# Performance work log

Measured on AMD Instinct MI355X. Metric: run time of the kernel, lower is better.

Reference implementation:

```python
import jax, jax.numpy as jnp
import numpy as np

H = 8        # heads
DH = 64      # dim_head
EPS = 1e-5   # LayerNorm eps (torch default)


def setup_inputs() -> dict:
    key = jax.random.key(0)
    k0, k1, k2, k3, k4 = jax.random.split(key, 5)
    b, l, n, dim = 2, 8, 256, 512
    inner = H * DH
    return {
        "xyzs": jax.random.normal(k0, (b, l, n, 3), dtype=jnp.float32),
        "features": jax.random.normal(k1, (b, l, n, dim), dtype=jnp.float32),
        "ln_gamma": jnp.ones((dim,), dtype=jnp.float32),
        "ln_beta": jnp.zeros((dim,), dtype=jnp.float32),
        "w_qkv": jax.random.normal(k2, (dim, 3 * inner), dtype=jnp.float32) * 0.02,
        "w_sp": jax.random.normal(k3, (3, DH), dtype=jnp.float32) * 0.3,
        "w_out": jax.random.normal(k4, (inner, dim), dtype=jnp.float32) * 0.02,
        "b_out": jnp.zeros((dim,), dtype=jnp.float32),
    }


def reference(xyzs, features, ln_gamma, ln_beta, w_qkv, w_sp, w_out, b_out):
    b, l, n, dim = features.shape
    m = l * n
    inner = H * DH
    scale = DH ** (-0.5)

    # LayerNorm over last dim (biased variance, eps=1e-5)
    mu = jnp.mean(features, axis=-1, keepdims=True)
    var = jnp.var(features, axis=-1, keepdims=True)
    normed = (features - mu) * jax.lax.rsqrt(var + EPS) * ln_gamma + ln_beta

    # qkv projection, chunk into q,k,v, reshape 'b l n (h d) -> b h (l n) d'
    qkv = normed.reshape(b, m, dim) @ w_qkv            # [b, m, 3*inner]
    def split_heads(t):
        return t.reshape(b, m, H, DH).transpose(0, 2, 1, 3)  # [b, h, m, d]
    q = split_heads(qkv[..., :inner])
    k = split_heads(qkv[..., inner:2 * inner])
    v = split_heads(qkv[..., 2 * inner:])

    dots = jnp.einsum('bhid,bhjd->bhij', q, k) * scale  # [b, h, m, m]
    attn = jax.nn.softmax(dots, axis=-1)
    v_out = jnp.einsum('bhij,bhjd->bhid', attn, v)      # [b, h, m, d]

    # pairwise coordinate deltas: delta[b,i,j,c] = xyz[b,j,c] - xyz[b,i,c]
    xyz_f = xyzs.reshape(b, m, 3)
    delta = xyz_f[:, None, :, :] - xyz_f[:, :, None, :]  # [b, m, m, 3]
    # attention-weighted aggregation over j (avoids [b,h,m,m,3] intermediate)
    agg = jnp.einsum('bhij,bijc->bhic', attn, delta)     # [b, h, m, 3]
    disp = agg @ w_sp                                    # [b, h, m, DH]

    out = v_out + disp                                   # [b, h, m, DH]
    out = out.transpose(0, 2, 1, 3).reshape(b, m, inner) # 'b h m d -> b m (h d)'
    out = jax.nn.gelu(out @ w_out + b_out, approximate=False)
    return out.reshape(b, l, n, dim) + features
```

## Files before the change

kernel.cpp:

```cpp
#include <hip/hip_runtime.h>
#include <hip/hip_bf16.h>
#include <math.h>

#define BB   2
#define MM   2048
#define DIM  512
#define NH   8
#define DHd  64
#define NQK  1536
#define ROWS 4096
#define NROW 32768

typedef __hip_bfloat16 bf16;
typedef __attribute__((ext_vector_type(8))) short bf16x8;
typedef __attribute__((ext_vector_type(4))) float f32x4;
typedef __attribute__((ext_vector_type(8))) unsigned short us8;

__device__ __forceinline__ unsigned short f2bf_bits(float x) {
    bf16 h = __float2bfloat16(x);
    return *(unsigned short*)&h;
}
__device__ __forceinline__ float bf2f(unsigned short u) {
    unsigned int v = ((unsigned int)u) << 16;
    return __uint_as_float(v);
}

__global__ __launch_bounds__(256) void pre_kernel(
    const float* __restrict__ feat, const float* __restrict__ gamma,
    const float* __restrict__ beta, unsigned short* __restrict__ normed,
    const float* __restrict__ wqkv, const float* __restrict__ wout,
    unsigned short* __restrict__ wqkvT, unsigned short* __restrict__ woutT)
{
    __shared__ float st[64][65];
    int b = blockIdx.x;
    int tid = threadIdx.x;
    if (b < ROWS) {
        const float* fr = feat + (size_t)b * DIM;
        float x0 = fr[tid];
        float x1 = fr[tid + 256];
        float s  = x0 + x1;
        float ss = x0 * x0 + x1 * x1;
        #pragma unroll
        for (int o = 32; o >= 1; o >>= 1) { s += __shfl_down(s, o); ss += __shfl_down(ss, o); }
        __shared__ float ws_[4], wss_[4];
        int wid = tid >> 6, lane = tid & 63;
        if (lane == 0) { ws_[wid] = s; wss_[wid] = ss; }
        __syncthreads();
        if (tid == 0) {
            float a = 0.f, c = 0.f;
            for (int i = 0; i < 4; i++) { a += ws_[i]; c += wss_[i]; }
            ws_[0] = a; wss_[0] = c;
        }
        __syncthreads();
        float mu  = ws_[0] * (1.0f / DIM);
        float var = wss_[0] * (1.0f / DIM) - mu * mu;
        float inv = rsqrtf(var + 1e-5f);
        normed[(size_t)b * DIM + tid]       = f2bf_bits((x0 - mu) * inv * gamma[tid] + beta[tid]);
        normed[(size_t)b * DIM + tid + 256] = f2bf_bits((x1 - mu) * inv * gamma[tid + 256] + beta[tid + 256]);
        return;
    }
    int idx = b - ROWS;
    const float* in; unsigned short* out; int N, n0;
    if (idx < 192) { in = wqkv; out = wqkvT; N = NQK; n0 = (idx >> 3) * 64; }
    else { idx -= 192; in = wout; out = woutT; N = DIM; n0 = (idx >> 3) * 64; }
    int k0 = (idx & 7) * 64;
    #pragma unroll
    for (int p = 0; p < 16; p++) {
        int e = tid + p * 256;
        int r = e >> 6, c = e & 63;
        st[r][c] = in[(size_t)(k0 + r) * N + n0 + c];
    }
    __syncthreads();
    #pragma unroll
    for (int p = 0; p < 16; p++) {
        int e = tid + p * 256;
        int nr = e >> 6, kc = e & 63;
        out[(size_t)(n0 + nr) * DIM + k0 + kc] = f2bf_bits(st[kc][nr]);
    }
}

__global__ __launch_bounds__(256) void qkv_gemm(
    const unsigned short* __restrict__ A, const unsigned short* __restrict__ BT,
    unsigned short* __restrict__ qd, unsigned short* __restrict__ kd,
    unsigned short* __restrict__ vd)
{
    __shared__ __align__(16) unsigned short sA[128 * 40];
    __shared__ __align__(16) unsigned short sB[128 * 40];
    int tid = threadIdx.x;
    int r0 = blockIdx.x * 128;
    int n0 = blockIdx.y * 128;
    int chunk = n0 >> 9;
    int cl    = n0 & 511;
    int w = tid >> 6, lane = tid & 63;
    int wm = w >> 1, wn = w & 1;
    int ln15 = lane & 15, quad = lane >> 4;

    int srow = tid >> 1;
    int scol = (tid & 1) * 16;

    f32x4 acc[4][4] = {};

    for (int k0 = 0; k0 < DIM; k0 += 32) {
        __syncthreads();
        *(us8*)&sA[srow * 40 + scol]     = *(const us8*)&A[(size_t)(r0 + srow) * DIM + k0 + scol];
        *(us8*)&sA[srow * 40 + scol + 8] = *(const us8*)&A[(size_t)(r0 + srow) * DIM + k0 + scol + 8];
        *(us8*)&sB[srow * 40 + scol]     = *(const us8*)&BT[(size_t)(n0 + srow) * DIM + k0 + scol];
        *(us8*)&sB[srow * 40 + scol + 8] = *(const us8*)&BT[(size_t)(n0 + srow) * DIM + k0 + scol + 8];
        __syncthreads();
        const unsigned short* fa = (chunk == 2) ? sA : sB;
        const unsigned short* fb = (chunk == 2) ? sB : sA;
        bf16x8 af[4], bf_[4];
        #pragma unroll
        for (int i = 0; i < 4; i++)
            af[i] = *(const bf16x8*)&fa[(wm * 64 + i * 16 + ln15) * 40 + quad * 8];
        #pragma unroll
        for (int j = 0; j < 4; j++)
            bf_[j] = *(const bf16x8*)&fb[(wn * 64 + j * 16 + ln15) * 40 + quad * 8];
        #pragma unroll
        for (int i = 0; i < 4; i++)
            #pragma unroll
            for (int j = 0; j < 4; j++)
                acc[i][j] = __builtin_amdgcn_mfma_f32_16x16x32_bf16(af[i], bf_[j], acc[i][j], 0, 0, 0);
    }

    if (chunk == 2) {
        int rowb = r0 + wm * 64 + quad * 4;
        #pragma unroll
        for (int j = 0; j < 4; j++) {
            int c = cl + wn * 64 + j * 16 + ln15;
            int h = c >> 6, d = c & 63;
            #pragma unroll
            for (int i = 0; i < 4; i++) {
                int gr = rowb + i * 16;
                int bb = gr >> 11, mm = gr & 2047;
                ushort4 pk;
                pk.x = f2bf_bits(acc[i][j][0]);
                pk.y = f2bf_bits(acc[i][j][1]);
                pk.z = f2bf_bits(acc[i][j][2]);
                pk.w = f2bf_bits(acc[i][j][3]);
                *(ushort4*)&vd[((size_t)(bb * NH + h) * DHd + d) * MM + mm] = pk;
            }
        }
    } else {
        unsigned short* dst = (chunk == 0) ? qd : kd;
        float sc = (chunk == 0) ? 0.125f : 1.0f;
        #pragma unroll
        for (int i = 0; i < 4; i++) {
            int within0 = cl + wm * 64 + i * 16 + quad * 4;
            int h = within0 >> 6, d = within0 & 63;
            #pragma unroll
            for (int j = 0; j < 4; j++) {
                int gr = r0 + wn * 64 + j * 16 + ln15;
                int bb = gr >> 11, mm = gr & 2047;
                ushort4 pk;
                pk.x = f2bf_bits(acc[i][j][0] * sc);
                pk.y = f2bf_bits(acc[i][j][1] * sc);
                pk.z = f2bf_bits(acc[i][j][2] * sc);
                pk.w = f2bf_bits(acc[i][j][3] * sc);
                *(ushort4*)&dst[((size_t)(bb * NH + h) * MM + mm) * DHd + d] = pk;
            }
        }
    }
}

__global__ __launch_bounds__(256) void attn_kernel(
    const unsigned short* __restrict__ qg, const unsigned short* __restrict__ kg,
    const unsigned short* __restrict__ vg, const float* __restrict__ xyzs,
    unsigned short* __restrict__ obuf, float* __restrict__ lbuf)
{
    __shared__ __align__(16) unsigned short sQ[64 * 72];
    __shared__ __align__(16) unsigned short sK[64 * 72];
    __shared__ __align__(16) unsigned short sVT[80 * 72];
    __shared__ __align__(16) unsigned short sP[64 * 72];

    int tid = threadIdx.x;
    int bh = blockIdx.y; int bb = bh >> 3;
    int i0 = blockIdx.x * 64;
    int ks = blockIdx.z;
    int w = tid >> 6;
    int lane = tid & 63;
    int ln15 = lane & 15;
    int quad = lane >> 4;

    for (int e = tid; e < 12 * 72; e += 256) sVT[68 * 72 + e] = 0;
    if (tid < 64) sVT[67 * 72 + tid] = 0x3F80;

    {
        const unsigned short* src = qg + ((size_t)bh * MM + i0) * DHd;
        int row = tid >> 2, col = (tid & 3) * 16;
        *(us8*)&sQ[row * 72 + col]     = *(const us8*)&src[(size_t)tid * 16];
        *(us8*)&sQ[row * 72 + col + 8] = *(const us8*)&src[(size_t)tid * 16 + 8];
    }
    asm volatile("s_waitcnt lgkmcnt(0)" ::: "memory");
    bf16x8 aq0 = *(const bf16x8*)&sQ[(w * 16 + ln15) * 72 + quad * 8];
    bf16x8 aq1 = *(const bf16x8*)&sQ[(w * 16 + ln15) * 72 + 32 + quad * 8];

    f32x4 o[5] = {};

    const unsigned short* kbase = kg + (size_t)bh * MM * DHd;
    const unsigned short* vbase = vg + (size_t)bh * DHd * MM;
    int jbeg = ks * (MM / 2), jend = jbeg + (MM / 2);

    int srow = tid >> 2, scol16 = (tid & 3) * 16;

    us8 rk0, rk1, rv0, rv1;
    float rx = 0.f;
    {
        const unsigned short* src = kbase + (size_t)jbeg * DHd;
        rk0 = *(const us8*)&src[(size_t)tid * 16];
        rk1 = *(const us8*)&src[(size_t)tid * 16 + 8];
        const unsigned short* vs = vbase + jbeg;
        rv0 = *(const us8*)&vs[(size_t)srow * MM + scol16];
        rv1 = *(const us8*)&vs[(size_t)srow * MM + scol16 + 8];
        if (tid < 192) rx = xyzs[((size_t)bb * MM + jbeg) * 3 + tid];
    }

    int pwb = quad << 4;
    int swzr = (ln15 >> 2) << 4;
    int pr0 = (quad * 8) ^ swzr;
    int pr1 = (32 + quad * 8) ^ swzr;

    for (int jt = jbeg; jt < jend; jt += 64) {
        __syncthreads();
        *(us8*)&sK[srow * 72 + scol16]      = rk0;
        *(us8*)&sK[srow * 72 + scol16 + 8]  = rk1;
        *(us8*)&sVT[srow * 72 + scol16]     = rv0;
        *(us8*)&sVT[srow * 72 + scol16 + 8] = rv1;
        if (tid < 192) {
            int key = tid / 3, c = tid - key * 3;
            sVT[(64 + c) * 72 + key] = f2bf_bits(rx);
        }
        __syncthreads();
        int jn = jt + 64;
        if (jn < jend) {
            const unsigned short* src = kbase + (size_t)jn * DHd;
            rk0 = *(const us8*)&src[(size_t)tid * 16];
            rk1 = *(const us8*)&src[(size_t)tid * 16 + 8];
            const unsigned short* vs = vbase + jn;
            rv0 = *(const us8*)&vs[(size_t)srow * MM + scol16];
            rv1 = *(const us8*)&vs[(size_t)srow * MM + scol16 + 8];
            if (tid < 192) rx = xyzs[((size_t)bb * MM + jn) * 3 + tid];
        }

        f32x4 sacc[4];
        #pragma unroll
        for (int t = 0; t < 4; t++) {
            bf16x8 bk0 = *(const bf16x8*)&sK[(t * 16 + ln15) * 72 + quad * 8];
            bf16x8 bk1 = *(const bf16x8*)&sK[(t * 16 + ln15) * 72 + 32 + quad * 8];
            f32x4 z = {};
            z = __builtin_amdgcn_mfma_f32_16x16x32_bf16(aq0, bk0, z, 0, 0, 0);
            z = __builtin_amdgcn_mfma_f32_16x16x32_bf16(aq1, bk1, z, 0, 0, 0);
            sacc[t] = z;
        }

        #pragma unroll
        for (int t = 0; t < 4; t++) {
            int colb = (t * 16) ^ pwb;
            #pragma unroll
            for (int reg = 0; reg < 4; reg++) {
                float pv = __expf(sacc[t][reg]);
                sP[(w * 16 + quad * 4 + reg) * 72 + colb + ln15] = f2bf_bits(pv);
            }
        }
        asm volatile("s_waitcnt lgkmcnt(0)" ::: "memory");
        bf16x8 ap0 = *(const bf16x8*)&sP[(w * 16 + ln15) * 72 + pr0];
        bf16x8 ap1 = *(const bf16x8*)&sP[(w * 16 + ln15) * 72 + pr1];
        #pragma unroll
        for (int t = 0; t < 5; t++) {
            bf16x8 bv0 = *(const bf16x8*)&sVT[(t * 16 + ln15) * 72 + quad * 8];
            bf16x8 bv1 = *(const bf16x8*)&sVT[(t * 16 + ln15) * 72 + 32 + quad * 8];
            o[t] = __builtin_amdgcn_mfma_f32_16x16x32_bf16(ap0, bv0, o[t], 0, 0, 0);
            o[t] = __builtin_amdgcn_mfma_f32_16x16x32_bf16(ap1, bv1, o[t], 0, 0, 0);
        }
    }

    size_t kso = (size_t)ks * NROW;
    #pragma unroll
    for (int reg = 0; reg < 4; reg++) {
        size_t row = (size_t)bh * MM + i0 + w * 16 + quad * 4 + reg;
        unsigned short* orow = obuf + (kso + row) * 72;
        #pragma unroll
        for (int t = 0; t < 4; t++)
            orow[t * 16 + ln15] = f2bf_bits(o[t][reg]);
        if (ln15 < 3)  orow[64 + ln15] = f2bf_bits(o[4][reg]);
        if (ln15 == 3) lbuf[kso + row] = o[4][reg];
    }
}

__global__ __launch_bounds__(256) void merge_kernel(
    const unsigned short* __restrict__ obuf, const float* __restrict__ lbuf,
    const float* __restrict__ xyzs, const float* __restrict__ wsp,
    unsigned short* __restrict__ attn_out)
{
    __shared__ float sW[3][64];
    int tid = threadIdx.x;
    if (tid < 192) sW[tid >> 6][tid & 63] = wsp[tid];
    __syncthreads();
    int r   = blockIdx.x * 64 + (tid >> 2);
    int d0  = (tid & 3) * 16;
    int bh = r >> 11, qrow = r & 2047, bb = bh >> 3, hh = bh & 7;
    const unsigned short* p1 = obuf + (size_t)r * 72;
    const unsigned short* p2 = obuf + ((size_t)NROW + r) * 72;
    float invl = 1.f / (lbuf[r] + lbuf[NROW + r]);
    size_t xb = ((size_t)bb * MM + qrow) * 3;
    float gx = (bf2f(p1[64]) + bf2f(p2[64])) * invl - xyzs[xb + 0];
    float gy = (bf2f(p1[65]) + bf2f(p2[65])) * invl - xyzs[xb + 1];
    float gz = (bf2f(p1[66]) + bf2f(p2[66])) * invl - xyzs[xb + 2];
    us8 a0 = *(const us8*)&p1[d0];
    us8 a1 = *(const us8*)&p1[d0 + 8];
    us8 b0 = *(const us8*)&p2[d0];
    us8 b1 = *(const us8*)&p2[d0 + 8];
    unsigned short outv[16];
    #pragma unroll
    for (int e = 0; e < 8; e++) {
        int d = d0 + e;
        float v = (bf2f(a0[e]) + bf2f(b0[e])) * invl
                + gx * sW[0][d] + gy * sW[1][d] + gz * sW[2][d];
        outv[e] = f2bf_bits(v);
    }
    #pragma unroll
    for (int e = 0; e < 8; e++) {
        int d = d0 + 8 + e;
        float v = (bf2f(a1[e]) + bf2f(b1[e])) * invl
                + gx * sW[0][d] + gy * sW[1][d] + gz * sW[2][d];
        outv[8 + e] = f2bf_bits(v);
    }
    unsigned short* dst = attn_out + ((size_t)bb * MM + qrow) * DIM + hh * DHd + d0;
    *(us8*)dst       = *(us8*)&outv[0];
    *(us8*)(dst + 8) = *(us8*)&outv[8];
}

__global__ __launch_bounds__(256) void out_gemm(
    const unsigned short* __restrict__ A, const unsigned short* __restrict__ BT,
    const float* __restrict__ bias, const float* __restrict__ feat,
    float* __restrict__ out)
{
    __shared__ __align__(16) unsigned short sA[64 * 40];
    __shared__ __align__(16) unsigned short sB[64 * 40];
    int tid = threadIdx.x;
    int r0 = blockIdx.x * 64, n0 = blockIdx.y * 64;
    int w = tid >> 6, lane = tid & 63;
    int wm = w >> 1, wn = w & 1;
    int ln15 = lane & 15, quad = lane >> 4;

    int srow = tid >> 2, scol = (tid & 3) * 8;

    f32x4 acc[2][2] = {};

    for (int k0 = 0; k0 < DIM; k0 += 32) {
        __syncthreads();
        *(us8*)&sA[srow * 40 + scol] = *(const us8*)&A[(size_t)(r0 + srow) * DIM + k0 + scol];
        *(us8*)&sB[srow * 40 + scol] = *(const us8*)&BT[(size_t)(n0 + srow) * DIM + k0 + scol];
        __syncthreads();
        bf16x8 af[2], bf_[2];
        #pragma unroll
        for (int i = 0; i < 2; i++)
            af[i] = *(const bf16x8*)&sA[(wm * 32 + i * 16 + ln15) * 40 + quad * 8];
        #pragma unroll
        for (int j = 0; j < 2; j++)
            bf_[j] = *(const bf16x8*)&sB[(wn * 32 + j * 16 + ln15) * 40 + quad * 8];
        #pragma unroll
        for (int i = 0; i < 2; i++)
            #pragma unroll
            for (int j = 0; j < 2; j++)
                acc[i][j] = __builtin_amdgcn_mfma_f32_16x16x32_bf16(af[i], bf_[j], acc[i][j], 0, 0, 0);
    }

    #pragma unroll
    for (int i = 0; i < 2; i++) {
        #pragma unroll
        for (int reg = 0; reg < 4; reg++) {
            int gr = r0 + wm * 32 + i * 16 + quad * 4 + reg;
            #pragma unroll
            for (int j = 0; j < 2; j++) {
                int c = n0 + wn * 32 + j * 16 + ln15;
                float x = acc[i][j][reg] + bias[c];
                float g = 0.5f * x * (1.f + erff(x * 0.70710678118f));
                out[(size_t)gr * DIM + c] = g + feat[(size_t)gr * DIM + c];
            }
        }
    }
}

extern "C" void kernel_launch(void* const* d_in, const int* in_sizes, int n_in,
                              void* d_out, int out_size, void* d_ws, size_t ws_size,
                              hipStream_t stream)
{
    const float* xyzs  = (const float*)d_in[0];
    const float* feat  = (const float*)d_in[1];
    const float* gamma = (const float*)d_in[2];
    const float* beta  = (const float*)d_in[3];
    const float* wqkv  = (const float*)d_in[4];
    const float* wsp   = (const float*)d_in[5];
    const float* wout  = (const float*)d_in[6];
    const float* bout  = (const float*)d_in[7];
    float* out = (float*)d_out;

    unsigned short* ws16 = (unsigned short*)d_ws;
    const size_t SEGS = (size_t)ROWS * DIM;
    unsigned short* normed = ws16;
    unsigned short* qb     = ws16 + SEGS;
    unsigned short* kb     = ws16 + 2 * SEGS;
    unsigned short* vb     = ws16 + 3 * SEGS;
    unsigned short* wqkvT  = ws16 + 4 * SEGS;
    unsigned short* woutT  = wqkvT + (size_t)NQK * DIM;
    unsigned short* obuf   = woutT + (size_t)DIM * DIM;
    float*          lbuf   = (float*)(obuf + (size_t)2 * NROW * 72);

    pre_kernel<<<ROWS + 256, 256, 0, stream>>>(feat, gamma, beta, normed,
                                               wqkv, wout, wqkvT, woutT);
    qkv_gemm<<<dim3(32, 12), 256, 0, stream>>>(normed, wqkvT, qb, kb, vb);
    attn_kernel<<<dim3(32, 16, 2), 256, 0, stream>>>(qb, kb, vb, xyzs, obuf, lbuf);
    merge_kernel<<<512, 256, 0, stream>>>(obuf, lbuf, xyzs, wsp, normed);
    out_gemm<<<dim3(64, 8), 256, 0, stream>>>(normed, woutT, bout, feat, out);
}
```

Baseline: 154.1 us.

## Double query rows per attention block and split keys four ways

Each attention block now processes 128 query rows (32 per wave, two 16-row fragments), so every K/V tile loaded into shared memory is reused by twice as many MFMA operations. Q is loaded straight from global memory into registers, removing the sQ staging buffer. Keys are split four ways instead of two to keep the grid size unchanged, and the merge kernel now sums four partial outputs. The cost is more registers per wave under a 4-blocks-per-CU launch bound, plus a larger partial buffer that the merge step must read.

```diff
diff --git a/kernel.cpp b/kernel.cpp
--- a/kernel.cpp
+++ b/kernel.cpp
@@ -10,6 +10,7 @@
 #define NQK  1536
 #define ROWS 4096
 #define NROW 32768
+#define SPLITK 4
 
 typedef __hip_bfloat16 bf16;
 typedef __attribute__((ext_vector_type(8))) short bf16x8;
@@ -163,19 +164,18 @@
     }
 }
 
-__global__ __launch_bounds__(256) void attn_kernel(
+__global__ __launch_bounds__(256, 4) void attn_kernel(
     const unsigned short* __restrict__ qg, const unsigned short* __restrict__ kg,
     const unsigned short* __restrict__ vg, const float* __restrict__ xyzs,
     unsigned short* __restrict__ obuf, float* __restrict__ lbuf)
 {
-    __shared__ __align__(16) unsigned short sQ[64 * 72];
     __shared__ __align__(16) unsigned short sK[64 * 72];
     __shared__ __align__(16) unsigned short sVT[80 * 72];
-    __shared__ __align__(16) unsigned short sP[64 * 72];
+    __shared__ __align__(16) unsigned short sP[128 * 72];
 
     int tid = threadIdx.x;
     int bh = blockIdx.y; int bb = bh >> 3;
-    int i0 = blockIdx.x * 64;
+    int i0 = blockIdx.x * 128;
     int ks = blockIdx.z;
     int w = tid >> 6;
     int lane = tid & 63;
@@ -185,21 +185,20 @@
     for (int e = tid; e < 12 * 72; e += 256) sVT[68 * 72 + e] = 0;
     if (tid < 64) sVT[67 * 72 + tid] = 0x3F80;
 
+    bf16x8 aq[2][2];
     {
-        const unsigned short* src = qg + ((size_t)bh * MM + i0) * DHd;
-        int row = tid >> 2, col = (tid & 3) * 16;
-        *(us8*)&sQ[row * 72 + col]     = *(const us8*)&src[(size_t)tid * 16];
-        *(us8*)&sQ[row * 72 + col + 8] = *(const us8*)&src[(size_t)tid * 16 + 8];
-    }
-    asm volatile("s_waitcnt lgkmcnt(0)" ::: "memory");
-    bf16x8 aq0 = *(const bf16x8*)&sQ[(w * 16 + ln15) * 72 + quad * 8];
-    bf16x8 aq1 = *(const bf16x8*)&sQ[(w * 16 + ln15) * 72 + 32 + quad * 8];
-
-    f32x4 o[5] = {};
+        const unsigned short* q0 = qg + ((size_t)bh * MM + i0 + w * 32 + ln15) * DHd + quad * 8;
+        aq[0][0] = *(const bf16x8*)q0;
+        aq[0][1] = *(const bf16x8*)(q0 + 32);
+        aq[1][0] = *(const bf16x8*)(q0 + 16 * DHd);
+        aq[1][1] = *(const bf16x8*)(q0 + 16 * DHd + 32);
+    }
+
+    f32x4 o[2][5] = {};
 
     const unsigned short* kbase = kg + (size_t)bh * MM * DHd;
     const unsigned short* vbase = vg + (size_t)bh * DHd * MM;
-    int jbeg = ks * (MM / 2), jend = jbeg + (MM / 2);
+    int jbeg = ks * (MM / SPLITK), jend = jbeg + (MM / SPLITK);
 
     int srow = tid >> 2, scol16 = (tid & 3) * 16;
 
@@ -242,48 +241,54 @@
             if (tid < 192) rx = xyzs[((size_t)bb * MM + jn) * 3 + tid];
         }
 
-        f32x4 sacc[4];
         #pragma unroll
         for (int t = 0; t < 4; t++) {
             bf16x8 bk0 = *(const bf16x8*)&sK[(t * 16 + ln15) * 72 + quad * 8];
             bf16x8 bk1 = *(const bf16x8*)&sK[(t * 16 + ln15) * 72 + 32 + quad * 8];
-            f32x4 z = {};
-            z = __builtin_amdgcn_mfma_f32_16x16x32_bf16(aq0, bk0, z, 0, 0, 0);
-            z = __builtin_amdgcn_mfma_f32_16x16x32_bf16(aq1, bk1, z, 0, 0, 0);
-            sacc[t] = z;
-        }
-
-        #pragma unroll
-        for (int t = 0; t < 4; t++) {
             int colb = (t * 16) ^ pwb;
             #pragma unroll
-            for (int reg = 0; reg < 4; reg++) {
-                float pv = __expf(sacc[t][reg]);
-                sP[(w * 16 + quad * 4 + reg) * 72 + colb + ln15] = f2bf_bits(pv);
+            for (int rf = 0; rf < 2; rf++) {
+                f32x4 z = {};
+                z = __builtin_amdgcn_mfma_f32_16x16x32_bf16(aq[rf][0], bk0, z, 0, 0, 0);
+                z = __builtin_amdgcn_mfma_f32_16x16x32_bf16(aq[rf][1], bk1, z, 0, 0, 0);
+                int rbase = (w * 32 + rf * 16 + quad * 4) * 72 + colb + ln15;
+                sP[rbase]           = f2bf_bits(__expf(z[0]));
+                sP[rbase + 72]      = f2bf_bits(__expf(z[1]));
+                sP[rbase + 144]     = f2bf_bits(__expf(z[2]));
+                sP[rbase + 216]     = f2bf_bits(__expf(z[3]));
             }
         }
         asm volatile("s_waitcnt lgkmcnt(0)" ::: "memory");
-        bf16x8 ap0 = *(const bf16x8*)&sP[(w * 16 + ln15) * 72 + pr0];
-        bf16x8 ap1 = *(const bf16x8*)&sP[(w * 16 + ln15) * 72 + pr1];
+        bf16x8 ap[2][2];
+        ap[0][0] = *(const bf16x8*)&sP[(w * 32 + ln15) * 72 + pr0];
+        ap[0][1] = *(const bf16x8*)&sP[(w * 32 + ln15) * 72 + pr1];
+        ap[1][0] = *(const bf16x8*)&sP[(w * 32 + 16 + ln15) * 72 + pr0];
+        ap[1][1] = *(const bf16x8*)&sP[(w * 32 + 16 + ln15) * 72 + pr1];
         #pragma unroll
         for (int t = 0; t < 5; t++) {
             bf16x8 bv0 = *(const bf16x8*)&sVT[(t * 16 + ln15) * 72 + quad * 8];
             bf16x8 bv1 = *(const bf16x8*)&sVT[(t * 16 + ln15) * 72 + 32 + quad * 8];
-            o[t] = __builtin_amdgcn_mfma_f32_16x16x32_bf16(ap0, bv0, o[t], 0, 0, 0);
-            o[t] = __builtin_amdgcn_mfma_f32_16x16x32_bf16(ap1, bv1, o[t], 0, 0, 0);
+            #pragma unroll
+            for (int rf = 0; rf < 2; rf++) {
+                o[rf][t] = __builtin_amdgcn_mfma_f32_16x16x32_bf16(ap[rf][0], bv0, o[rf][t], 0, 0, 0);
+                o[rf][t] = __builtin_amdgcn_mfma_f32_16x16x32_bf16(ap[rf][1], bv1, o[rf][t], 0, 0, 0);
+            }
         }
     }
 
     size_t kso = (size_t)ks * NROW;
     #pragma unroll
-    for (int reg = 0; reg < 4; reg++) {
-        size_t row = (size_t)bh * MM + i0 + w * 16 + quad * 4 + reg;
-        unsigned short* orow = obuf + (kso + row) * 72;
-        #pragma unroll
-        for (int t = 0; t < 4; t++)
-            orow[t * 16 + ln15] = f2bf_bits(o[t][reg]);
-        if (ln15 < 3)  orow[64 + ln15] = f2bf_bits(o[4][reg]);
-        if (ln15 == 3) lbuf[kso + row] = o[4][reg];
+    for (int rf = 0; rf < 2; rf++) {
+        #pragma unroll
+        for (int reg = 0; reg < 4; reg++) {
+            size_t row = (size_t)bh * MM + i0 + w * 32 + rf * 16 + quad * 4 + reg;
+            unsigned short* orow = obuf + (kso + row) * 72;
+            #pragma unroll
+            for (int t = 0; t < 4; t++)
+                orow[t * 16 + ln15] = f2bf_bits(o[rf][t][reg]);
+            if (ln15 < 3)  orow[64 + ln15] = f2bf_bits(o[rf][4][reg]);
+            if (ln15 == 3) lbuf[kso + row] = o[rf][4][reg];
+        }
     }
 }
 
@@ -299,29 +304,35 @@
     int r   = blockIdx.x * 64 + (tid >> 2);
     int d0  = (tid & 3) * 16;
     int bh = r >> 11, qrow = r & 2047, bb = bh >> 3, hh = bh & 7;
-    const unsigned short* p1 = obuf + (size_t)r * 72;
-    const unsigned short* p2 = obuf + ((size_t)NROW + r) * 72;
-    float invl = 1.f / (lbuf[r] + lbuf[NROW + r]);
+    const unsigned short* p0 = obuf + (size_t)r * 72;
+    const unsigned short* p1 = p0 + (size_t)NROW * 72;
+    const unsigned short* p2 = p1 + (size_t)NROW * 72;
+    const unsigned short* p3 = p2 + (size_t)NROW * 72;
+    float invl = 1.f / (lbuf[r] + lbuf[NROW + r] + lbuf[2 * NROW + r] + lbuf[3 * NROW + r]);
     size_t xb = ((size_t)bb * MM + qrow) * 3;
-    float gx = (bf2f(p1[64]) + bf2f(p2[64])) * invl - xyzs[xb + 0];
-    float gy = (bf2f(p1[65]) + bf2f(p2[65])) * invl - xyzs[xb + 1];
-    float gz = (bf2f(p1[66]) + bf2f(p2[66])) * invl - xyzs[xb + 2];
-    us8 a0 = *(const us8*)&p1[d0];
-    us8 a1 = *(const us8*)&p1[d0 + 8];
-    us8 b0 = *(const us8*)&p2[d0];
-    us8 b1 = *(const us8*)&p2[d0 + 8];
+    float gx = (bf2f(p0[64]) + bf2f(p1[64]) + bf2f(p2[64]) + bf2f(p3[64])) * invl - xyzs[xb + 0];
+    float gy = (bf2f(p0[65]) + bf2f(p1[65]) + bf2f(p2[65]) + bf2f(p3[65])) * invl - xyzs[xb + 1];
+    float gz = (bf2f(p0[66]) + bf2f(p1[66]) + bf2f(p2[66]) + bf2f(p3[66])) * invl - xyzs[xb + 2];
+    us8 a0 = *(const us8*)&p0[d0];
+    us8 a1 = *(const us8*)&p0[d0 + 8];
+    us8 b0 = *(const us8*)&p1[d0];
+    us8 b1 = *(const us8*)&p1[d0 + 8];
+    us8 c0 = *(const us8*)&p2[d0];
+    us8 c1 = *(const us8*)&p2[d0 + 8];
+    us8 e0 = *(const us8*)&p3[d0];
+    us8 e1 = *(const us8*)&p3[d0 + 8];
     unsigned short outv[16];
     #pragma unroll
     for (int e = 0; e < 8; e++) {
         int d = d0 + e;
-        float v = (bf2f(a0[e]) + bf2f(b0[e])) * invl
+        float v = (bf2f(a0[e]) + bf2f(b0[e]) + bf2f(c0[e]) + bf2f(e0[e])) * invl
                 + gx * sW[0][d] + gy * sW[1][d] + gz * sW[2][d];
         outv[e] = f2bf_bits(v);
     }
     #pragma unroll
     for (int e = 0; e < 8; e++) {
         int d = d0 + 8 + e;
-        float v = (bf2f(a1[e]) + bf2f(b1[e])) * invl
+        float v = (bf2f(a1[e]) + bf2f(b1[e]) + bf2f(c1[e]) + bf2f(e1[e])) * invl
                 + gx * sW[0][d] + gy * sW[1][d] + gz * sW[2][d];
         outv[8 + e] = f2bf_bits(v);
     }
@@ -405,12 +416,12 @@
     unsigned short* wqkvT  = ws16 + 4 * SEGS;
     unsigned short* woutT  = wqkvT + (size_t)NQK * DIM;
     unsigned short* obuf   = woutT + (size_t)DIM * DIM;
-    float*          lbuf   = (float*)(obuf + (size_t)2 * NROW * 72);
+    float*          lbuf   = (float*)(obuf + (size_t)SPLITK * NROW * 72);
 
     pre_kernel<<<ROWS + 256, 256, 0, stream>>>(feat, gamma, beta, normed,
                                                wqkv, wout, wqkvT, woutT);
     qkv_gemm<<<dim3(32, 12), 256, 0, stream>>>(normed, wqkvT, qb, kb, vb);
-    attn_kernel<<<dim3(32, 16, 2), 256, 0, stream>>>(qb, kb, vb, xyzs, obuf, lbuf);
+    attn_kernel<<<dim3(16, 16, SPLITK), 256, 0, stream>>>(qb, kb, vb, xyzs, obuf, lbuf);
     merge_kernel<<<512, 256, 0, stream>>>(obuf, lbuf, xyzs, wsp, normed);
     out_gemm<<<dim3(64, 8), 256, 0, stream>>>(normed, woutT, bout, feat, out);
 }
```

Result: faster. 150.1 us (-2.6%).
